# Kernel tuning notes

Hardware: AMD Instinct MI355X
Metric: run time of the kernel (lower is better)

## Reference

```python
import jax, jax.numpy as jnp
import numpy as np

N, A, C = 2048, 256, 100   # batch, feat_dim, num_classes
LAT = A // 2               # latent_dim = feat_dim // 2
BN_EPS = 1e-5


def setup_inputs() -> dict:
    key = jax.random.key(0)
    ks = jax.random.split(key, 8)
    s = jax.random.normal(ks[0], (N, A), dtype=jnp.float32)
    y = jax.random.randint(ks[1], (N,), 0, C)
    ratio = jnp.float32(0.5)
    W1 = jax.random.normal(ks[2], (LAT, A), dtype=jnp.float32) / np.sqrt(A)
    b1 = jnp.zeros((LAT,), jnp.float32)
    gamma = jnp.ones((LAT,), jnp.float32)
    beta = jnp.zeros((LAT,), jnp.float32)
    W2 = jax.random.normal(ks[3], (A, LAT), dtype=jnp.float32) / np.sqrt(LAT)
    b2 = jnp.zeros((A,), jnp.float32)
    Wfc = jax.random.normal(ks[4], (C, A), dtype=jnp.float32) / np.sqrt(A)
    bfc = jnp.zeros((C,), jnp.float32)
    # per-class covariance table [C, A, A], symmetric PSD like a real EstimatorCV state
    M = jax.random.normal(ks[5], (C, A, A), dtype=jnp.float32)
    cov = jnp.einsum('cab,cdb->cad', M, M) / A
    return {"s": s, "y": y, "ratio": ratio, "W1": W1, "b1": b1,
            "gamma": gamma, "beta": beta, "W2": W2, "b2": b2,
            "Wfc": Wfc, "bfc": bfc, "cov": cov}


def reference(s, y, ratio, W1, b1, gamma, beta, W2, b2, Wfc, bfc, cov):
    # pred: Linear -> BatchNorm1d (train-mode batch stats) -> ReLU -> Linear -> ReLU
    h = s @ W1.T + b1                                   # [N, LAT]
    mu = jnp.mean(h, axis=0)
    var = jnp.var(h, axis=0)                            # biased, as torch BN
    h = (h - mu) / jnp.sqrt(var + BN_EPS) * gamma + beta
    h = jax.nn.relu(h)
    f = jax.nn.relu(h @ W2.T + b2)                      # [N, A]
    z = f @ Wfc.T + bfc                                 # [N, C]

    # correct_z: diag of (W_i - W_y) cov[y] (W_i - W_y)^T, computed without the
    # wasted off-diagonal bmm of the original
    cov_sg = jax.lax.stop_gradient(cov)                 # cov is detached in source
    Wy = Wfc[y]                                         # [N, A]
    diff = Wfc[None, :, :] - Wy[:, None, :]             # [N, C, A]
    CVy = cov_sg[y]                                     # [N, A, A]
    tmp = jnp.einsum('nca,nab->ncb', diff, CVy)         # [N, C, A]
    sigma2 = jnp.sum(tmp * diff, axis=-1)               # [N, C] = diag of quad form
    return z + ratio * 0.5 * sigma2
```

## Files before the change

### kernel.cpp

```cpp
#include <hip/hip_runtime.h>
#include <hip/hip_bf16.h>

#define Nn  2048
#define Aa  256
#define Cc  100
#define LAT 128
#define BN_EPS 1e-5f

#define OFF_HB   0
#define OFF_SUMS (OFF_HB + Nn*LAT/2)
#define OFF_SP   (OFF_SUMS + 128*256)
#define OFF_W2B  (OFF_SP + 2*Cc*Cc)
#define OFF_WFB  (OFF_W2B + Aa*LAT/2)

typedef __attribute__((ext_vector_type(8))) short bf16x8;
typedef __attribute__((ext_vector_type(4))) float f32x4;

__device__ __forceinline__ short f2bf(float f) {
    return (short)__bfloat16_as_ushort(__float2bfloat16(f));
}
__device__ __forceinline__ float bf2f(short h) {
    return __uint_as_float(((unsigned)(unsigned short)h) << 16);
}

#define DPITCH 264
#define FPITCH 264
#define NWG_A  530

template<int MSZ>
__device__ __forceinline__ void ks_body(
    const float* __restrict__ Wfc, const float* __restrict__ cov,
    float* __restrict__ Spart, short* Dlds, float (*red)[64],
    int k, int ch, int bh, int t, int w, int il, int q)
{
    const float* covk = cov + (size_t)k * (Aa * Aa);
    const int c0 = ch * 64;

    {
        const int c4 = t & 63;
        float4 wk = *(const float4*)&Wfc[(size_t)k * Aa + c4 * 4];
#pragma unroll
        for (int j = 0; j < MSZ * 4; j++) {
            int row = (t >> 6) + j * 4;
            int g = c0 + row;
            short4 o = {0, 0, 0, 0};
            if (g < Cc) {
                float4 v = *(const float4*)&Wfc[(size_t)g * Aa + c4 * 4];
                o.x = f2bf(v.x - wk.x); o.y = f2bf(v.y - wk.y);
                o.z = f2bf(v.z - wk.z); o.w = f2bf(v.w - wk.w);
            }
            *(short4*)&Dlds[row * DPITCH + c4 * 4] = o;
        }
    }
    __syncthreads();

    const int bbase = bh * 128 + w * 32;

    f32x4 acc[MSZ][2];
#pragma unroll
    for (int m = 0; m < MSZ; m++) {
        acc[m][0] = (f32x4){0.f,0.f,0.f,0.f};
        acc[m][1] = (f32x4){0.f,0.f,0.f,0.f};
    }

    const float* brow0 = covk + (size_t)(bbase + il) * Aa;
    const float* brow1 = covk + (size_t)(bbase + 16 + il) * Aa;

    float4 p0a = *(const float4*)&brow0[q * 8];
    float4 p0b = *(const float4*)&brow0[q * 8 + 4];
    float4 p1a = *(const float4*)&brow1[q * 8];
    float4 p1b = *(const float4*)&brow1[q * 8 + 4];

#pragma unroll
    for (int sgk = 0; sgk < 8; sgk++) {
        const float4 c0a = p0a, c0b = p0b, c1a = p1a, c1b = p1b;
        if (sgk < 7) {
            const int a1 = (sgk + 1) * 32 + q * 8;
            p0a = *(const float4*)&brow0[a1];
            p0b = *(const float4*)&brow0[a1 + 4];
            p1a = *(const float4*)&brow1[a1];
            p1b = *(const float4*)&brow1[a1 + 4];
        }
        const int a0 = sgk * 32 + q * 8;
        bf16x8 bm0, bm1;
        bm0[0]=f2bf(c0a.x); bm0[1]=f2bf(c0a.y); bm0[2]=f2bf(c0a.z); bm0[3]=f2bf(c0a.w);
        bm0[4]=f2bf(c0b.x); bm0[5]=f2bf(c0b.y); bm0[6]=f2bf(c0b.z); bm0[7]=f2bf(c0b.w);
        bm1[0]=f2bf(c1a.x); bm1[1]=f2bf(c1a.y); bm1[2]=f2bf(c1a.z); bm1[3]=f2bf(c1a.w);
        bm1[4]=f2bf(c1b.x); bm1[5]=f2bf(c1b.y); bm1[6]=f2bf(c1b.z); bm1[7]=f2bf(c1b.w);
#pragma unroll
        for (int m = 0; m < MSZ; m++) {
            bf16x8 am = *(bf16x8*)&Dlds[(m * 16 + il) * DPITCH + a0];
            acc[m][0] = __builtin_amdgcn_mfma_f32_16x16x32_bf16(am, bm0, acc[m][0], 0, 0, 0);
            acc[m][1] = __builtin_amdgcn_mfma_f32_16x16x32_bf16(am, bm1, acc[m][1], 0, 0, 0);
        }
    }

#pragma unroll
    for (int m = 0; m < MSZ; m++) {
        float sacc[4] = {0.f, 0.f, 0.f, 0.f};
#pragma unroll
        for (int nf = 0; nf < 2; nf++) {
            int bcol = bbase + nf * 16 + il;
#pragma unroll
            for (int r = 0; r < 4; r++) {
                int crow = m * 16 + q * 4 + r;
                float dv = bf2f(Dlds[crow * DPITCH + bcol]);
                sacc[r] = fmaf(dv, acc[m][nf][r], sacc[r]);
            }
        }
#pragma unroll
        for (int r = 0; r < 4; r++) {
            float v = sacc[r];
            v += __shfl_xor(v, 1);
            v += __shfl_xor(v, 2);
            v += __shfl_xor(v, 4);
            v += __shfl_xor(v, 8);
            if (il == 0) red[w][m * 16 + q * 4 + r] = v;
        }
    }
    __syncthreads();
    if (t < MSZ * 16) {
        int c = c0 + t;
        if (c < Cc)
            Spart[bh * (Cc * Cc) + k * Cc + c] =
                red[0][t] + red[1][t] + red[2][t] + red[3][t];
    }
}

__global__ __launch_bounds__(256) void kA(
    const float* __restrict__ s, const float* __restrict__ W1,
    const float* __restrict__ b1, const float* __restrict__ Wfc,
    const float* __restrict__ W2, const float* __restrict__ cov,
    short* __restrict__ hB, float* __restrict__ sums, float* __restrict__ Spart,
    short* __restrict__ W2b, short* __restrict__ Wfcb)
{
    __shared__ __align__(16) char smem[64 * DPITCH * 2 + 4 * 64 * 4];
    const int orig = blockIdx.x;
    const int xcd  = orig % 8;
    const int bid  = (xcd < 2 ? xcd * 67 : 2 * 67 + (xcd - 2) * 66) + orig / 8;
    const int t = threadIdx.x;
    const int w = t >> 6, l = t & 63, il = l & 15, q = l >> 4;

    if (bid < 400) {
        short* Dlds = (short*)smem;
        float (*red)[64] = (float(*)[64])(smem + 64 * DPITCH * 2);
        const int k  = bid >> 2;
        const int ch = (bid >> 1) & 1;
        const int bh = bid & 1;
        if (ch == 0)
            ks_body<4>(Wfc, cov, Spart, Dlds, red, k, 0, bh, t, w, il, q);
        else
            ks_body<3>(Wfc, cov, Spart, Dlds, red, k, 1, bh, t, w, il, q);
    } else if (bid < 528) {
        const int bid2 = bid - 400;
        const int row0 = bid2 * 16;
        const int colw = w * 32;

        f32x4 acc[2];
        acc[0] = (f32x4){0.f,0.f,0.f,0.f};
        acc[1] = (f32x4){0.f,0.f,0.f,0.f};

        const float* arow = s  + (size_t)(row0 + il) * Aa;
        const float* bp0  = W1 + (size_t)(colw + il) * Aa;
        const float* bp1  = W1 + (size_t)(colw + 16 + il) * Aa;

        float4 pu0 = *(const float4*)&arow[q * 8];
        float4 pu1 = *(const float4*)&arow[q * 8 + 4];
        float4 pv0 = *(const float4*)&bp0[q * 8];
        float4 pv1 = *(const float4*)&bp0[q * 8 + 4];
        float4 px0 = *(const float4*)&bp1[q * 8];
        float4 px1 = *(const float4*)&bp1[q * 8 + 4];

#pragma unroll
        for (int ks = 0; ks < 8; ks++) {
            const float4 u0 = pu0, u1 = pu1, v0 = pv0, v1 = pv1, x0 = px0, x1 = px1;
            if (ks < 7) {
                const int k1n = (ks + 1) * 32 + q * 8;
                pu0 = *(const float4*)&arow[k1n];
                pu1 = *(const float4*)&arow[k1n + 4];
                pv0 = *(const float4*)&bp0[k1n];
                pv1 = *(const float4*)&bp0[k1n + 4];
                px0 = *(const float4*)&bp1[k1n];
                px1 = *(const float4*)&bp1[k1n + 4];
            }
            bf16x8 am;
            am[0]=f2bf(u0.x); am[1]=f2bf(u0.y); am[2]=f2bf(u0.z); am[3]=f2bf(u0.w);
            am[4]=f2bf(u1.x); am[5]=f2bf(u1.y); am[6]=f2bf(u1.z); am[7]=f2bf(u1.w);
            bf16x8 bm0;
            bm0[0]=f2bf(v0.x); bm0[1]=f2bf(v0.y); bm0[2]=f2bf(v0.z); bm0[3]=f2bf(v0.w);
            bm0[4]=f2bf(v1.x); bm0[5]=f2bf(v1.y); bm0[6]=f2bf(v1.z); bm0[7]=f2bf(v1.w);
            bf16x8 bm1;
            bm1[0]=f2bf(x0.x); bm1[1]=f2bf(x0.y); bm1[2]=f2bf(x0.z); bm1[3]=f2bf(x0.w);
            bm1[4]=f2bf(x1.x); bm1[5]=f2bf(x1.y); bm1[6]=f2bf(x1.z); bm1[7]=f2bf(x1.w);
            acc[0] = __builtin_amdgcn_mfma_f32_16x16x32_bf16(am, bm0, acc[0], 0, 0, 0);
            acc[1] = __builtin_amdgcn_mfma_f32_16x16x32_bf16(am, bm1, acc[1], 0, 0, 0);
        }

#pragma unroll
        for (int n = 0; n < 2; n++) {
            const int col = colw + n * 16 + il;
            const float bias = b1[col];
            float s1 = 0.f, s2 = 0.f;
#pragma unroll
            for (int r = 0; r < 4; r++) {
                float v = acc[n][r] + bias;
                hB[(size_t)(row0 + q * 4 + r) * LAT + col] = f2bf(v);
                s1 += v; s2 += v * v;
            }
            s1 += __shfl_xor(s1, 16); s1 += __shfl_xor(s1, 32);
            s2 += __shfl_xor(s2, 16); s2 += __shfl_xor(s2, 32);
            if (q == 0) {
                sums[bid2 * 256 + col]       = s1;
                sums[bid2 * 256 + 128 + col] = s2;
            }
        }
    } else if (bid == 528) {
        for (int i = t * 4; i < Aa * LAT; i += 1024) {
            float4 v = *(const float4*)&W2[i];
            short4 o = {f2bf(v.x), f2bf(v.y), f2bf(v.z), f2bf(v.w)};
            *(short4*)&W2b[i] = o;
        }
    } else {
        for (int i = t * 4; i < 128 * Aa; i += 1024) {
            int row = i >> 8;
            short4 o = {0, 0, 0, 0};
            if (row < Cc) {
                float4 v = *(const float4*)&Wfc[i];
                o.x = f2bf(v.x); o.y = f2bf(v.y); o.z = f2bf(v.z); o.w = f2bf(v.w);
            }
            *(short4*)&Wfcb[i] = o;
        }
    }
}

__global__ __launch_bounds__(256) void kB(
    const short* __restrict__ hB, const float* __restrict__ sums,
    const float* __restrict__ gamma, const float* __restrict__ beta,
    const short* __restrict__ W2b, const float* __restrict__ b2,
    const short* __restrict__ Wfcb, const float* __restrict__ bfc,
    const float* __restrict__ Spart, const int* __restrict__ y,
    const float* __restrict__ ratio, float* __restrict__ out)
{
    __shared__ float scL[LAT], shL[LAT];
    __shared__ short fLDS[16 * FPITCH];
    const int t = threadIdx.x;
    const int w = t >> 6, l = t & 63, il = l & 15, q = l >> 4;
    const int row0 = blockIdx.x * 16;

    if (t < 128) {
        float a1 = 0.f, a2 = 0.f;
#pragma unroll 8
        for (int b = 0; b < 128; b++) {
            a1 += sums[b * 256 + t];
            a2 += sums[b * 256 + 128 + t];
        }
        float mu  = a1 * (1.0f / Nn);
        float var = a2 * (1.0f / Nn) - mu * mu;
        float inv = rsqrtf(var + BN_EPS);
        float sc  = gamma[t] * inv;
        scL[t] = sc;
        shL[t] = beta[t] - mu * sc;
    }
    __syncthreads();

    f32x4 acc3[4];
#pragma unroll
    for (int n = 0; n < 4; n++) acc3[n] = (f32x4){0.f,0.f,0.f,0.f};

    const short* arow = hB + (size_t)(row0 + il) * LAT;
#pragma unroll
    for (int ks = 0; ks < 4; ks++) {
        const int k0 = ks * 32 + q * 8;
        bf16x8 ha = *(const bf16x8*)&arow[k0];
        bf16x8 am;
#pragma unroll
        for (int j = 0; j < 8; j++) {
            float fv = fmaf(bf2f(ha[j]), scL[k0 + j], shL[k0 + j]);
            am[j] = f2bf(fmaxf(fv, 0.f));
        }
#pragma unroll
        for (int n = 0; n < 4; n++) {
            const int col = w * 64 + n * 16 + il;
            bf16x8 bm = *(const bf16x8*)&W2b[(size_t)col * LAT + k0];
            acc3[n] = __builtin_amdgcn_mfma_f32_16x16x32_bf16(am, bm, acc3[n], 0, 0, 0);
        }
    }
#pragma unroll
    for (int n = 0; n < 4; n++) {
        const int col = w * 64 + n * 16 + il;
        const float bias = b2[col];
#pragma unroll
        for (int r = 0; r < 4; r++) {
            float v = fmaxf(acc3[n][r] + bias, 0.f);
            fLDS[(q * 4 + r) * FPITCH + col] = f2bf(v);
        }
    }
    __syncthreads();

    f32x4 acc4[2];
    acc4[0] = (f32x4){0.f,0.f,0.f,0.f};
    acc4[1] = (f32x4){0.f,0.f,0.f,0.f};
#pragma unroll
    for (int ks = 0; ks < 8; ks++) {
        const int k0 = ks * 32 + q * 8;
        bf16x8 am = *(const bf16x8*)&fLDS[il * FPITCH + k0];
#pragma unroll
        for (int n = 0; n < 2; n++) {
            const int col = w * 32 + n * 16 + il;
            bf16x8 bm = *(const bf16x8*)&Wfcb[(size_t)col * Aa + k0];
            acc4[n] = __builtin_amdgcn_mfma_f32_16x16x32_bf16(am, bm, acc4[n], 0, 0, 0);
        }
    }

    const float coef = 0.5f * ratio[0];
    const int4 yv4 = *(const int4*)&y[row0 + q * 4];
    const int yr[4] = {yv4.x, yv4.y, yv4.z, yv4.w};

#pragma unroll
    for (int n = 0; n < 2; n++) {
        const int col = w * 32 + n * 16 + il;
        if (col < Cc) {
            const float bias = bfc[col];
#pragma unroll
            for (int r = 0; r < 4; r++) {
                const float* sp = &Spart[yr[r] * Cc + col];
                float sv = sp[0] + sp[Cc * Cc];
                out[(size_t)(row0 + q * 4 + r) * Cc + col] =
                    acc4[n][r] + bias + coef * sv;
            }
        }
    }
}

extern "C" void kernel_launch(void* const* d_in, const int* in_sizes, int n_in,
                              void* d_out, int out_size, void* d_ws, size_t ws_size,
                              hipStream_t stream)
{
    const float* s     = (const float*)d_in[0];
    const int*   y     = (const int*)  d_in[1];
    const float* ratio = (const float*)d_in[2];
    const float* W1    = (const float*)d_in[3];
    const float* b1    = (const float*)d_in[4];
    const float* gamma = (const float*)d_in[5];
    const float* beta  = (const float*)d_in[6];
    const float* W2    = (const float*)d_in[7];
    const float* b2    = (const float*)d_in[8];
    const float* Wfc   = (const float*)d_in[9];
    const float* bfc   = (const float*)d_in[10];
    const float* cov   = (const float*)d_in[11];
    float* out = (float*)d_out;
    float* ws  = (float*)d_ws;

    short* hB    = (short*)(ws + OFF_HB);
    float* sums  = ws + OFF_SUMS;
    float* Spart = ws + OFF_SP;
    short* W2b   = (short*)(ws + OFF_W2B);
    short* Wfcb  = (short*)(ws + OFF_WFB);

    hipLaunchKernelGGL(kA, dim3(NWG_A), dim3(256), 0, stream,
                       s, W1, b1, Wfc, W2, cov, hB, sums, Spart, W2b, Wfcb);
    hipLaunchKernelGGL(kB, dim3(128), dim3(256), 0, stream,
                       hB, sums, gamma, beta, W2b, b2, Wfcb, bfc, Spart, y, ratio, out);
}
```

Baseline: 34.83 us.

## Stage covariance tiles through LDS with coalesced loads and split BN-stat reduction

The per-class covariance kernel body now loads cov rows with fully coalesced float4 reads, converts them to bf16 and writes them into an LDS tile. Each 32-row chunk is double-buffered in registers while MFMAs read B fragments from LDS. The old path had each lane gather strided 8-float segments straight from global memory. Separately, kB's batch-norm statistic reduction now uses all 256 threads, splitting the 128 partial rows in halves and combining them through shared memory. The cost is extra LDS, additional barriers per chunk, and a different k-split layout of the MFMA accumulation.

Result: faster. 31.29 us, median of 2 (-10.2%).

```diff
diff --git a/kernel.cpp b/kernel.cpp
--- a/kernel.cpp
+++ b/kernel.cpp
@@ -27,14 +27,19 @@
 #define FPITCH 264
 #define NWG_A  530
 
+#define KS_DBYTES   (64 * DPITCH * 2)
+#define KS_CBYTES   (32 * DPITCH * 2)
+#define KS_SMEM     (KS_DBYTES + KS_CBYTES + 4 * 64 * 4)
+
 template<int MSZ>
-__device__ __forceinline__ void ks_body(
+__device__ __forceinline__ void ks_body2(
     const float* __restrict__ Wfc, const float* __restrict__ cov,
-    float* __restrict__ Spart, short* Dlds, float (*red)[64],
+    float* __restrict__ Spart, short* Dlds, short* covT, float (*red)[64],
     int k, int ch, int bh, int t, int w, int il, int q)
 {
     const float* covk = cov + (size_t)k * (Aa * Aa);
     const int c0 = ch * 64;
+    const int lane = t & 63;
 
     {
         const int c4 = t & 63;
@@ -52,65 +57,78 @@
             *(short4*)&Dlds[row * DPITCH + c4 * 4] = o;
         }
     }
-    __syncthreads();
-
-    const int bbase = bh * 128 + w * 32;
-
-    f32x4 acc[MSZ][2];
+
+    float4 pre[8];
+#pragma unroll
+    for (int i = 0; i < 8; i++)
+        pre[i] = *(const float4*)&covk[(size_t)(bh * 128 + w * 8 + i) * Aa + lane * 4];
+
+    __syncthreads();
+#pragma unroll
+    for (int i = 0; i < 8; i++) {
+        short4 o = {f2bf(pre[i].x), f2bf(pre[i].y), f2bf(pre[i].z), f2bf(pre[i].w)};
+        *(short4*)&covT[(w * 8 + i) * DPITCH + lane * 4] = o;
+    }
+    __syncthreads();
+
+    float sacc[MSZ][4];
+#pragma unroll
+    for (int m = 0; m < MSZ; m++)
+#pragma unroll
+        for (int r = 0; r < 4; r++) sacc[m][r] = 0.f;
+
+    for (int p = 0; p < 4; p++) {
+        if (p < 3) {
+#pragma unroll
+            for (int i = 0; i < 8; i++)
+                pre[i] = *(const float4*)&covk[(size_t)(bh * 128 + (p + 1) * 32 + w * 8 + i) * Aa + lane * 4];
+        }
+
+        f32x4 acc[MSZ][2];
+#pragma unroll
+        for (int m = 0; m < MSZ; m++) {
+            acc[m][0] = (f32x4){0.f,0.f,0.f,0.f};
+            acc[m][1] = (f32x4){0.f,0.f,0.f,0.f};
+        }
+#pragma unroll
+        for (int sg = 0; sg < 2; sg++) {
+            const int a0 = w * 64 + sg * 32 + q * 8;
+            bf16x8 bm0 = *(bf16x8*)&covT[il * DPITCH + a0];
+            bf16x8 bm1 = *(bf16x8*)&covT[(16 + il) * DPITCH + a0];
+#pragma unroll
+            for (int m = 0; m < MSZ; m++) {
+                bf16x8 am = *(bf16x8*)&Dlds[(m * 16 + il) * DPITCH + a0];
+                acc[m][0] = __builtin_amdgcn_mfma_f32_16x16x32_bf16(am, bm0, acc[m][0], 0, 0, 0);
+                acc[m][1] = __builtin_amdgcn_mfma_f32_16x16x32_bf16(am, bm1, acc[m][1], 0, 0, 0);
+            }
+        }
+#pragma unroll
+        for (int m = 0; m < MSZ; m++)
+#pragma unroll
+            for (int nf = 0; nf < 2; nf++) {
+                const int bcol = bh * 128 + p * 32 + nf * 16 + il;
+#pragma unroll
+                for (int r = 0; r < 4; r++) {
+                    float dv = bf2f(Dlds[(m * 16 + q * 4 + r) * DPITCH + bcol]);
+                    sacc[m][r] = fmaf(dv, acc[m][nf][r], sacc[m][r]);
+                }
+            }
+        __syncthreads();
+        if (p < 3) {
+#pragma unroll
+            for (int i = 0; i < 8; i++) {
+                short4 o = {f2bf(pre[i].x), f2bf(pre[i].y), f2bf(pre[i].z), f2bf(pre[i].w)};
+                *(short4*)&covT[(w * 8 + i) * DPITCH + lane * 4] = o;
+            }
+            __syncthreads();
+        }
+    }
+
 #pragma unroll
     for (int m = 0; m < MSZ; m++) {
-        acc[m][0] = (f32x4){0.f,0.f,0.f,0.f};
-        acc[m][1] = (f32x4){0.f,0.f,0.f,0.f};
-    }
-
-    const float* brow0 = covk + (size_t)(bbase + il) * Aa;
-    const float* brow1 = covk + (size_t)(bbase + 16 + il) * Aa;
-
-    float4 p0a = *(const float4*)&brow0[q * 8];
-    float4 p0b = *(const float4*)&brow0[q * 8 + 4];
-    float4 p1a = *(const float4*)&brow1[q * 8];
-    float4 p1b = *(const float4*)&brow1[q * 8 + 4];
-
-#pragma unroll
-    for (int sgk = 0; sgk < 8; sgk++) {
-        const float4 c0a = p0a, c0b = p0b, c1a = p1a, c1b = p1b;
-        if (sgk < 7) {
-            const int a1 = (sgk + 1) * 32 + q * 8;
-            p0a = *(const float4*)&brow0[a1];
-            p0b = *(const float4*)&brow0[a1 + 4];
-            p1a = *(const float4*)&brow1[a1];
-            p1b = *(const float4*)&brow1[a1 + 4];
-        }
-        const int a0 = sgk * 32 + q * 8;
-        bf16x8 bm0, bm1;
-        bm0[0]=f2bf(c0a.x); bm0[1]=f2bf(c0a.y); bm0[2]=f2bf(c0a.z); bm0[3]=f2bf(c0a.w);
-        bm0[4]=f2bf(c0b.x); bm0[5]=f2bf(c0b.y); bm0[6]=f2bf(c0b.z); bm0[7]=f2bf(c0b.w);
-        bm1[0]=f2bf(c1a.x); bm1[1]=f2bf(c1a.y); bm1[2]=f2bf(c1a.z); bm1[3]=f2bf(c1a.w);
-        bm1[4]=f2bf(c1b.x); bm1[5]=f2bf(c1b.y); bm1[6]=f2bf(c1b.z); bm1[7]=f2bf(c1b.w);
-#pragma unroll
-        for (int m = 0; m < MSZ; m++) {
-            bf16x8 am = *(bf16x8*)&Dlds[(m * 16 + il) * DPITCH + a0];
-            acc[m][0] = __builtin_amdgcn_mfma_f32_16x16x32_bf16(am, bm0, acc[m][0], 0, 0, 0);
-            acc[m][1] = __builtin_amdgcn_mfma_f32_16x16x32_bf16(am, bm1, acc[m][1], 0, 0, 0);
-        }
-    }
-
-#pragma unroll
-    for (int m = 0; m < MSZ; m++) {
-        float sacc[4] = {0.f, 0.f, 0.f, 0.f};
-#pragma unroll
-        for (int nf = 0; nf < 2; nf++) {
-            int bcol = bbase + nf * 16 + il;
-#pragma unroll
-            for (int r = 0; r < 4; r++) {
-                int crow = m * 16 + q * 4 + r;
-                float dv = bf2f(Dlds[crow * DPITCH + bcol]);
-                sacc[r] = fmaf(dv, acc[m][nf][r], sacc[r]);
-            }
-        }
 #pragma unroll
         for (int r = 0; r < 4; r++) {
-            float v = sacc[r];
+            float v = sacc[m][r];
             v += __shfl_xor(v, 1);
             v += __shfl_xor(v, 2);
             v += __shfl_xor(v, 4);
@@ -134,7 +152,7 @@
     short* __restrict__ hB, float* __restrict__ sums, float* __restrict__ Spart,
     short* __restrict__ W2b, short* __restrict__ Wfcb)
 {
-    __shared__ __align__(16) char smem[64 * DPITCH * 2 + 4 * 64 * 4];
+    __shared__ __align__(16) char smem[KS_SMEM];
     const int orig = blockIdx.x;
     const int xcd  = orig % 8;
     const int bid  = (xcd < 2 ? xcd * 67 : 2 * 67 + (xcd - 2) * 66) + orig / 8;
@@ -143,14 +161,15 @@
 
     if (bid < 400) {
         short* Dlds = (short*)smem;
-        float (*red)[64] = (float(*)[64])(smem + 64 * DPITCH * 2);
+        short* covT = (short*)(smem + KS_DBYTES);
+        float (*red)[64] = (float(*)[64])(smem + KS_DBYTES + KS_CBYTES);
         const int k  = bid >> 2;
         const int ch = (bid >> 1) & 1;
         const int bh = bid & 1;
         if (ch == 0)
-            ks_body<4>(Wfc, cov, Spart, Dlds, red, k, 0, bh, t, w, il, q);
+            ks_body2<4>(Wfc, cov, Spart, Dlds, covT, red, k, 0, bh, t, w, il, q);
         else
-            ks_body<3>(Wfc, cov, Spart, Dlds, red, k, 1, bh, t, w, il, q);
+            ks_body2<3>(Wfc, cov, Spart, Dlds, covT, red, k, 1, bh, t, w, il, q);
     } else if (bid < 528) {
         const int bid2 = bid - 400;
         const int row0 = bid2 * 16;
@@ -242,20 +261,29 @@
     const float* __restrict__ ratio, float* __restrict__ out)
 {
     __shared__ float scL[LAT], shL[LAT];
+    __shared__ float redA[512];
     __shared__ short fLDS[16 * FPITCH];
     const int t = threadIdx.x;
     const int w = t >> 6, l = t & 63, il = l & 15, q = l >> 4;
     const int row0 = blockIdx.x * 16;
 
+    {
+        const int chn = t & 127, hf = t >> 7;
+        float a1 = 0.f, a2 = 0.f;
+#pragma unroll 16
+        for (int b = hf * 64; b < hf * 64 + 64; b++) {
+            a1 += sums[b * 256 + chn];
+            a2 += sums[b * 256 + 128 + chn];
+        }
+        redA[hf * 256 + chn]       = a1;
+        redA[hf * 256 + 128 + chn] = a2;
+    }
+    __syncthreads();
     if (t < 128) {
-        float a1 = 0.f, a2 = 0.f;
-#pragma unroll 8
-        for (int b = 0; b < 128; b++) {
-            a1 += sums[b * 256 + t];
-            a2 += sums[b * 256 + 128 + t];
-        }
-        float mu  = a1 * (1.0f / Nn);
-        float var = a2 * (1.0f / Nn) - mu * mu;
+        float A1 = redA[t] + redA[256 + t];
+        float A2 = redA[128 + t] + redA[384 + t];
+        float mu  = A1 * (1.0f / Nn);
+        float var = A2 * (1.0f / Nn) - mu * mu;
         float inv = rsqrtf(var + BN_EPS);
         float sc  = gamma[t] * inv;
         scL[t] = sc;
```
